# Performance work log

Hardware: AMD Instinct MI355X
Metric: run time of the kernel (lower is better)

The kernel has to match this reference:

```python
import jax, jax.numpy as jnp
import numpy as np

VOCAB = 32000
E = 512      # embed_dim
H = 512      # hidden_dim (== embed_dim, required by the output-averaging slice)
NUM_LAYERS = 2
WIN = 8
S = 512      # seq_len
B = 8        # batch


def setup_inputs() -> dict:
    key = jax.random.key(0)
    ks = jax.random.split(key, 40)
    d = {"encoder_input": jax.random.randint(ks[0], (S, B), 0, VOCAB, dtype=jnp.int64
                                             if jax.config.jax_enable_x64 else jnp.int32)}
    d["embed_table"] = jax.random.normal(ks[1], (VOCAB, E), jnp.float32) * 0.02
    i = 2
    for l in range(NUM_LAYERS):
        in_dim = E if l == 0 else 2 * H
        for dirn in ("f", "b"):
            sc = 1.0 / np.sqrt(H).astype(np.float32)
            d[f"wih{l}{dirn}"] = jax.random.normal(ks[i], (4 * H, in_dim), jnp.float32) * sc; i += 1
            d[f"whh{l}{dirn}"] = jax.random.normal(ks[i], (4 * H, H), jnp.float32) * sc; i += 1
            d[f"b{l}{dirn}"] = jax.random.normal(ks[i], (4 * H,), jnp.float32) * sc; i += 1
    return d


def _lstm_dir(x, mask, wih, whh, b, reverse):
    """One LSTM direction over padded windows. x: [L, N, in], mask: [L, N, 1].
    Masked (out-of-window) steps carry state unchanged; since invalid steps form a
    prefix in scan order (left pad for fwd, right pad for bwd-reversed), the zero
    initial state is preserved until the first valid step -> identical math to
    running the LSTM on the truncated window, as in the original per-token loop."""
    Hh = whh.shape[1]

    def step(carry, inp):
        h, c = carry
        xt, mt = inp
        g = xt @ wih.T + h @ whh.T + b                      # [N, 4H], torch gate order i,f,g,o
        i_, f_, g_, o_ = jnp.split(g, 4, axis=-1)
        c_new = jax.nn.sigmoid(f_) * c + jax.nn.sigmoid(i_) * jnp.tanh(g_)
        h_new = jax.nn.sigmoid(o_) * jnp.tanh(c_new)
        h = jnp.where(mt, h_new, h)
        c = jnp.where(mt, c_new, c)
        return (h, c), h

    N = x.shape[1]
    h0 = jnp.zeros((N, Hh), x.dtype)
    _, ys = jax.lax.scan(step, (h0, h0), (x, mask), reverse=reverse)
    return ys  # [L, N, Hh]


def _forward(encoder_input, embed_table, layer_params):
    S_, B_ = encoder_input.shape
    L = 2 * WIN + 1
    emb = embed_table[encoder_input]                         # [S, B, E]
    offs = jnp.arange(L) - WIN
    pos = jnp.arange(S_)[:, None] + offs[None, :]            # [S, L]
    valid = (pos >= 0) & (pos < S_)
    pidx = jnp.clip(pos, 0, S_ - 1)
    windows = emb[pidx]                                      # [S, L, B, E]
    x = windows.transpose(1, 0, 2, 3).reshape(L, S_ * B_, E)  # [L, N, E]
    mask = jnp.broadcast_to(valid.T[:, :, None, None], (L, S_, B_, 1)).reshape(L, S_ * B_, 1)
    for (wf, hf, bf, wb, hb, bb) in layer_params:
        yf = _lstm_dir(x, mask, wf, hf, bf, reverse=False)
        yb = _lstm_dir(x, mask, wb, hb, bb, reverse=True)
        x = jnp.concatenate([yf, yb], axis=-1)               # [L, N, 2H]
    out = x[WIN].reshape(S_, B_, 2 * H)                      # [S, B, 2H]
    return (out[:, :, :E] + out[:, :, E:]) / 2


def reference(encoder_input, embed_table,
              wih0f, whh0f, b0f, wih0b, whh0b, b0b,
              wih1f, whh1f, b1f, wih1b, whh1b, b1b):
    layer_params = [(wih0f, whh0f, b0f, wih0b, whh0b, b0b),
                    (wih1f, whh1f, b1f, wih1b, whh1b, b1b)]
    return _forward(encoder_input, embed_table, layer_params)
```

## Files before the change

### kernel.cpp

```cpp
#include <hip/hip_runtime.h>
#include <stdint.h>

typedef __bf16 bf16;
typedef __bf16 bf16x8 __attribute__((ext_vector_type(8)));
typedef __bf16 bf16x4 __attribute__((ext_vector_type(4)));
typedef float f32x4 __attribute__((ext_vector_type(4)));

#define WIN 8

__device__ __forceinline__ float sigm(float x) { return 1.0f / (1.0f + __expf(-x)); }
__device__ __forceinline__ float tanhfast(float x) { return 2.0f / (1.0f + __expf(-2.0f * x)) - 1.0f; }

__device__ __forceinline__ void gload16(const void* g, void* l) {
    __builtin_amdgcn_global_load_lds((const __attribute__((address_space(1))) void*)g,
                                     (__attribute__((address_space(3))) void*)l, 16, 0, 0);
}

struct StepArgs {
    const bf16* A1;
    const bf16* A2;
    const bf16* W;
    const float* bias;
    const bf16* P0;
    float* Cst;
    bf16* Hout;
    float* Hf32;
    const bf16* Hprev;
    int l;
    int firstStep;
};

template<int MODE>
__global__ __launch_bounds__(512, 2)
void step_pair(StepArgs fa, StepArgs ba) {
    const StepArgs a = blockIdx.z ? ba : fa;
    __shared__ alignas(16) char lds[131072];

    constexpr int SA1 = (MODE == 0) ? 512 : 1024;
    constexpr int SW  = (MODE == 2) ? 1536 : 512;
    constexpr int SH  = (MODE == 0) ? 2048 : (MODE == 1 ? 1024 : 512);
    constexpr int SHP = (MODE == 1) ? 1024 : 512;

    const int tid = threadIdx.x;
    const int w = tid >> 6;
    const int lane = tid & 63;
    const int wm = w >> 2, wn = w & 3;
    const int bx = blockIdx.x, by = blockIdx.y;
    const int rowBase = bx * 256;

    int KB;
    if (MODE == 0) KB = 8;
    else if (MODE == 1) KB = a.firstStep ? 0 : 8;
    else KB = a.firstStep ? 16 : 24;

    const int lq = lane >> 3;
    const int lc = lane & 7;
    const int swz = 8 * (lc ^ lq);

    const bf16* aP[4];
    const bf16* a2P[4];
    const bf16* bP[4];
#pragma unroll
    for (int q = 0; q < 4; ++q) {
        const int r = w * 32 + q * 8 + lq;
        const int n = rowBase + r;
        aP[q] = a.A1 ? (a.A1 + (size_t)n * SA1 + swz) : (const bf16*)0;
        if (MODE == 2) a2P[q] = a.A2 ? (a.A2 + (size_t)n * 512 + swz) : (const bf16*)0;
        int wr;
        if (MODE == 0) wr = by * 256 + r;
        else wr = ((r & 63) >> 4) * 512 + by * 64 + (r >> 6) * 16 + (r & 15);
        bP[q] = a.W + (size_t)wr * SW + swz;
    }

    const int l15 = lane & 15, l4 = lane >> 4;
    const int key = (l15 & 7) << 4;
    const int aBase = (wm * 128 + l15) * 128;
    const int bBase = (wn * 64 + l15) * 128;

    f32x4 acc[8][4];
    const f32x4 zf = {0.f, 0.f, 0.f, 0.f};
#pragma unroll
    for (int m = 0; m < 8; ++m)
#pragma unroll
        for (int n = 0; n < 4; ++n) acc[m][n] = zf;

    auto STAGE = [&](int buf, int kb) {
        char* Ad = lds + buf * 65536;
        char* Bd = Ad + 32768;
        const int ke = kb * 64;
        const int ldsOff0 = w * 32 * 128;
#pragma unroll
        for (int q = 0; q < 4; ++q) {
            const int ldsOff = ldsOff0 + q * 1024;
            const bf16* srcA;
            if (MODE == 2) srcA = (kb < 16) ? (aP[q] + ke) : (a2P[q] + (ke - 1024));
            else srcA = aP[q] + ke;
            gload16(srcA, Ad + ldsOff);
            gload16(bP[q] + ke, Bd + ldsOff);
        }
    };

    auto LDA4 = [&](bf16x8* d, const char* Ab, int mh, int ko) {
#pragma unroll
        for (int i = 0; i < 4; ++i)
            d[i] = *(const bf16x8*)(Ab + aBase + (mh * 4 + i) * 2048 + ko);
    };
    auto LDB4 = [&](bf16x8* d, const char* Bb, int ko) {
#pragma unroll
        for (int n = 0; n < 4; ++n)
            d[n] = *(const bf16x8*)(Bb + bBase + n * 2048 + ko);
    };
    auto MF16 = [&](const bf16x8* av, const bf16x8* bvv, int mh) {
#pragma unroll
        for (int i = 0; i < 4; ++i)
#pragma unroll
            for (int n = 0; n < 4; ++n)
                acc[mh * 4 + i][n] =
                    __builtin_amdgcn_mfma_f32_16x16x32_bf16(av[i], bvv[n], acc[mh * 4 + i][n], 0, 0, 0);
    };

    if (KB > 0) {
        STAGE(0, 0);
        for (int t = 0; t < KB; ++t) {
            const int cur = t & 1;
            if (t + 1 < KB) {
                STAGE(cur ^ 1, t + 1);
                asm volatile("s_waitcnt vmcnt(8)" ::: "memory");
            } else {
                asm volatile("s_waitcnt vmcnt(0)" ::: "memory");
            }
            __builtin_amdgcn_s_barrier();
            __builtin_amdgcn_sched_barrier(0);
            const char* Ab = lds + cur * 65536;
            const char* Bb = Ab + 32768;
            const int ko0 = (l4 * 16) ^ key;
            const int ko1 = (64 + l4 * 16) ^ key;
            bf16x8 a00[4], a10[4], a01[4], a11[4], b0[4], b1[4];

            LDA4(a00, Ab, 0, ko0); LDB4(b0, Bb, ko0);
            asm volatile("s_waitcnt lgkmcnt(0)" ::: "memory");
            __builtin_amdgcn_sched_barrier(0);
            LDA4(a10, Ab, 0, ko1); LDB4(b1, Bb, ko1);
            __builtin_amdgcn_s_setprio(1);
            MF16(a00, b0, 0);
            __builtin_amdgcn_s_setprio(0);

            asm volatile("s_waitcnt lgkmcnt(0)" ::: "memory");
            __builtin_amdgcn_sched_barrier(0);
            LDA4(a01, Ab, 1, ko0);
            __builtin_amdgcn_s_setprio(1);
            MF16(a10, b1, 0);
            __builtin_amdgcn_s_setprio(0);

            asm volatile("s_waitcnt lgkmcnt(0)" ::: "memory");
            __builtin_amdgcn_sched_barrier(0);
            LDA4(a11, Ab, 1, ko1);
            __builtin_amdgcn_s_setprio(1);
            MF16(a01, b0, 1);
            __builtin_amdgcn_s_setprio(0);

            asm volatile("s_waitcnt lgkmcnt(0)" ::: "memory");
            __builtin_amdgcn_sched_barrier(0);
            __builtin_amdgcn_s_setprio(1);
            MF16(a11, b1, 1);
            __builtin_amdgcn_s_setprio(0);
            __builtin_amdgcn_sched_barrier(0);
            __builtin_amdgcn_s_barrier();
        }
    }

    if (MODE == 0) {
#pragma unroll
        for (int m = 0; m < 8; ++m)
#pragma unroll
            for (int n = 0; n < 4; ++n) {
                const int col = by * 256 + wn * 64 + n * 16 + l15;
#pragma unroll
                for (int e = 0; e < 4; ++e) {
                    const int row = rowBase + wm * 128 + m * 16 + l4 * 4 + e;
                    a.Hout[(size_t)row * SH + col] = (bf16)acc[m][n][e];
                }
            }
        return;
    }

    const int u = by * 64 + wn * 16 + l15;
    const float bi = a.bias[u];
    const float bff = a.bias[512 + u];
    const float bg = a.bias[1024 + u];
    const float bo = a.bias[1536 + u];
#pragma unroll
    for (int m = 0; m < 8; ++m) {
#pragma unroll
        for (int e = 0; e < 4; ++e) {
            const int n = rowBase + wm * 128 + m * 16 + l4 * 4 + e;
            const int s = n >> 3;
            const int p = s + a.l - WIN;
            const bool valid = ((unsigned)p < 512u);
            float gi = acc[m][0][e] + bi;
            float gf = acc[m][1][e] + bff;
            float gg = acc[m][2][e] + bg;
            float go = acc[m][3][e] + bo;
            if (MODE == 1) {
                const int pc = p < 0 ? 0 : (p > 511 ? 511 : p);
                const size_t pr = (size_t)(pc * 8 + (n & 7)) * 2048;
                gi += (float)a.P0[pr + u];
                gf += (float)a.P0[pr + 512 + u];
                gg += (float)a.P0[pr + 1024 + u];
                go += (float)a.P0[pr + 1536 + u];
            }
            const float cold = a.firstStep ? 0.0f : a.Cst[(size_t)n * 512 + u];
            const float cnew = sigm(gf) * cold + sigm(gi) * tanhfast(gg);
            const float hnew = sigm(go) * tanhfast(cnew);
            float hv, cv;
            if (valid) { hv = hnew; cv = cnew; }
            else {
                hv = a.Hprev ? (float)a.Hprev[(size_t)n * SHP + u] : 0.0f;
                cv = cold;
            }
            a.Cst[(size_t)n * 512 + u] = cv;
            a.Hout[(size_t)n * SH + u] = (bf16)hv;
            if (a.Hf32) a.Hf32[(size_t)n * 512 + u] = hv;
        }
    }
}

__global__ void embed_kernel(const int* __restrict__ tok, const float* __restrict__ tbl,
                             bf16* __restrict__ X0) {
    const int n = blockIdx.x;
    const int t = tok[n];
    const float4 v = ((const float4*)(tbl + (size_t)t * 512))[threadIdx.x];
    bf16x4 o = {(bf16)v.x, (bf16)v.y, (bf16)v.z, (bf16)v.w};
    ((bf16x4*)(X0 + (size_t)n * 512))[threadIdx.x] = o;
}

__global__ void cvt_kernel(const float* __restrict__ src, bf16* __restrict__ dst, int n4) {
    const int i = blockIdx.x * 256 + threadIdx.x;
    if (i < n4) {
        const float4 v = ((const float4*)src)[i];
        bf16x4 o = {(bf16)v.x, (bf16)v.y, (bf16)v.z, (bf16)v.w};
        ((bf16x4*)dst)[i] = o;
    }
}

__global__ void build_w1_kernel(const float* __restrict__ wih, const float* __restrict__ whh,
                                bf16* __restrict__ dst) {
    const int r = blockIdx.x;
    for (int k = threadIdx.x; k < 1536; k += 256) {
        const float v = (k < 1024) ? wih[(size_t)r * 1024 + k] : whh[(size_t)r * 512 + (k - 1024)];
        dst[(size_t)r * 1536 + k] = (bf16)v;
    }
}

__global__ void combine_kernel(const float* __restrict__ hf, const float* __restrict__ hb,
                               float* __restrict__ out) {
    const int i = blockIdx.x * 256 + threadIdx.x;
    const float4 x = ((const float4*)hf)[i];
    const float4 y = ((const float4*)hb)[i];
    float4 r;
    r.x = (x.x + y.x) * 0.5f;
    r.y = (x.y + y.y) * 0.5f;
    r.z = (x.z + y.z) * 0.5f;
    r.w = (x.w + y.w) * 0.5f;
    ((float4*)out)[i] = r;
}

extern "C" void kernel_launch(void* const* d_in, const int* in_sizes, int n_in,
                              void* d_out, int out_size, void* d_ws, size_t ws_size,
                              hipStream_t stream) {
    (void)in_sizes; (void)n_in; (void)out_size;
    const int*   tok   = (const int*)d_in[0];
    const float* tbl   = (const float*)d_in[1];
    const float* wih0f = (const float*)d_in[2];
    const float* whh0f = (const float*)d_in[3];
    const float* b0f   = (const float*)d_in[4];
    const float* wih0b = (const float*)d_in[5];
    const float* whh0b = (const float*)d_in[6];
    const float* b0b   = (const float*)d_in[7];
    const float* wih1f = (const float*)d_in[8];
    const float* whh1f = (const float*)d_in[9];
    const float* b1f   = (const float*)d_in[10];
    const float* wih1b = (const float*)d_in[11];
    const float* whh1b = (const float*)d_in[12];
    const float* b1b   = (const float*)d_in[13];

    char* ws = (char*)d_ws;
    size_t off = 0;
    auto alloc = [&](size_t bytes) -> char* {
        char* p = ws + off;
        off += (bytes + 255) & ~(size_t)255;
        return p;
    };
    bf16* wih0f_b = (bf16*)alloc((size_t)2048 * 512 * 2);
    bf16* wih0b_b = (bf16*)alloc((size_t)2048 * 512 * 2);
    bf16* whh0f_b = (bf16*)alloc((size_t)2048 * 512 * 2);
    bf16* whh0b_b = (bf16*)alloc((size_t)2048 * 512 * 2);
    bf16* w1f_b   = (bf16*)alloc((size_t)2048 * 1536 * 2);
    bf16* w1b_b   = (bf16*)alloc((size_t)2048 * 1536 * 2);
    bf16* X0      = (bf16*)alloc((size_t)4096 * 512 * 2);
    bf16* P0f     = (bf16*)alloc((size_t)4096 * 2048 * 2);
    bf16* P0b     = (bf16*)alloc((size_t)4096 * 2048 * 2);
    bf16* X1      = (bf16*)alloc((size_t)17 * 4096 * 1024 * 2);
    float* c0f    = (float*)alloc((size_t)4096 * 512 * 4);
    float* c0b    = (float*)alloc((size_t)4096 * 512 * 4);
    bf16* h1f0    = (bf16*)alloc((size_t)4096 * 512 * 2);
    bf16* h1f1    = (bf16*)alloc((size_t)4096 * 512 * 2);
    bf16* h1b0    = (bf16*)alloc((size_t)4096 * 512 * 2);
    bf16* h1b1    = (bf16*)alloc((size_t)4096 * 512 * 2);
    float* hf32f  = (float*)alloc((size_t)4096 * 512 * 4);
    float* hf32b  = (float*)alloc((size_t)4096 * 512 * 4);
    if (off > ws_size) return;

    bf16* h1f[2] = {h1f0, h1f1};
    bf16* h1b[2] = {h1b0, h1b1};

    cvt_kernel<<<1024, 256, 0, stream>>>(wih0f, wih0f_b, 262144);
    cvt_kernel<<<1024, 256, 0, stream>>>(wih0b, wih0b_b, 262144);
    cvt_kernel<<<1024, 256, 0, stream>>>(whh0f, whh0f_b, 262144);
    cvt_kernel<<<1024, 256, 0, stream>>>(whh0b, whh0b_b, 262144);
    build_w1_kernel<<<2048, 256, 0, stream>>>(wih1f, whh1f, w1f_b);
    build_w1_kernel<<<2048, 256, 0, stream>>>(wih1b, whh1b, w1b_b);
    embed_kernel<<<4096, 128, 0, stream>>>(tok, tbl, X0);

    dim3 g(16, 8, 2), blk(512, 1, 1);

    {
        StepArgs f{}, b{};
        f.A1 = X0; f.W = wih0f_b; f.Hout = P0f;
        b = f; b.W = wih0b_b; b.Hout = P0b;
        step_pair<0><<<g, blk, 0, stream>>>(f, b);
    }

    const size_t SLOT = (size_t)4096 * 1024;

    for (int i = 0; i <= 16; ++i) {
        const int lf = i, lb = 16 - i;
        StepArgs f{}, b{};
        f.A1 = (lf == 0) ? (const bf16*)0 : X1 + (size_t)(lf - 1) * SLOT;
        f.W = whh0f_b; f.bias = b0f; f.P0 = P0f; f.Cst = c0f;
        f.Hout = X1 + (size_t)lf * SLOT; f.Hprev = f.A1;
        f.l = lf; f.firstStep = (lf == 0) ? 1 : 0;
        b.A1 = (lb == 16) ? (const bf16*)0 : X1 + (size_t)(lb + 1) * SLOT + 512;
        b.W = whh0b_b; b.bias = b0b; b.P0 = P0b; b.Cst = c0b;
        b.Hout = X1 + (size_t)lb * SLOT + 512; b.Hprev = b.A1;
        b.l = lb; b.firstStep = (lb == 16) ? 1 : 0;
        step_pair<1><<<g, blk, 0, stream>>>(f, b);
    }

    for (int i = 0; i <= 8; ++i) {
        const int lf = i, lb = 16 - i;
        StepArgs f{}, b{};
        f.A1 = X1 + (size_t)lf * SLOT;
        f.A2 = (i == 0) ? (const bf16*)0 : h1f[(i + 1) & 1];
        f.W = w1f_b; f.bias = b1f; f.Cst = c0f;
        f.Hout = h1f[i & 1]; f.Hf32 = (i == 8) ? hf32f : (float*)0;
        f.Hprev = f.A2;
        f.l = lf; f.firstStep = (i == 0) ? 1 : 0;
        b.A1 = X1 + (size_t)lb * SLOT;
        b.A2 = (i == 0) ? (const bf16*)0 : h1b[(i + 1) & 1];
        b.W = w1b_b; b.bias = b1b; b.Cst = c0b;
        b.Hout = h1b[i & 1]; b.Hf32 = (i == 8) ? hf32b : (float*)0;
        b.Hprev = b.A2;
        b.l = lb; b.firstStep = (i == 0) ? 1 : 0;
        step_pair<2><<<g, blk, 0, stream>>>(f, b);
    }

    combine_kernel<<<2048, 256, 0, stream>>>(hf32f, hf32b, (float*)d_out);
}
```

Before: 1.156 ms.

## Interleave next-tile global-to-LDS prefetch chunks across MFMA phases in GEMM main loop

Splits the per-iteration prefetch of the next K-tile into four chunks issued between the four MFMA phases, instead of one bulk stage followed by a partial wait. Each phase now loads only its own fragments, and the loop waits for all prefetches once at the end of the iteration. The aim is to overlap global loads with compute more evenly and to reduce register pressure from fragment buffers. The cost is extra workgroup barriers in every phase, which may add stalls.

```diff
diff --git a/kernel.cpp b/kernel.cpp
--- a/kernel.cpp
+++ b/kernel.cpp
@@ -84,87 +84,104 @@
 #pragma unroll
         for (int n = 0; n < 4; ++n) acc[m][n] = zf;
 
-    auto STAGE = [&](int buf, int kb) {
-        char* Ad = lds + buf * 65536;
-        char* Bd = Ad + 32768;
+    auto CHUNK = [&](char* Sd, int kb, int q) {
         const int ke = kb * 64;
-        const int ldsOff0 = w * 32 * 128;
-#pragma unroll
-        for (int q = 0; q < 4; ++q) {
-            const int ldsOff = ldsOff0 + q * 1024;
-            const bf16* srcA;
-            if (MODE == 2) srcA = (kb < 16) ? (aP[q] + ke) : (a2P[q] + (ke - 1024));
-            else srcA = aP[q] + ke;
-            gload16(srcA, Ad + ldsOff);
-            gload16(bP[q] + ke, Bd + ldsOff);
-        }
+        const int ldsOff = (w * 32 + q * 8) * 128;
+        const bf16* srcA;
+        if (MODE == 2) srcA = (kb < 16) ? (aP[q] + ke) : (a2P[q] + (ke - 1024));
+        else srcA = aP[q] + ke;
+        gload16(srcA, Sd + ldsOff);
+        gload16(bP[q] + ke, Sd + 32768 + ldsOff);
     };
 
-    auto LDA4 = [&](bf16x8* d, const char* Ab, int mh, int ko) {
-#pragma unroll
-        for (int i = 0; i < 4; ++i)
-            d[i] = *(const bf16x8*)(Ab + aBase + (mh * 4 + i) * 2048 + ko);
-    };
-    auto LDB4 = [&](bf16x8* d, const char* Bb, int ko) {
-#pragma unroll
-        for (int n = 0; n < 4; ++n)
-            d[n] = *(const bf16x8*)(Bb + bBase + n * 2048 + ko);
-    };
-    auto MF16 = [&](const bf16x8* av, const bf16x8* bvv, int mh) {
-#pragma unroll
-        for (int i = 0; i < 4; ++i)
-#pragma unroll
-            for (int n = 0; n < 4; ++n)
-                acc[mh * 4 + i][n] =
-                    __builtin_amdgcn_mfma_f32_16x16x32_bf16(av[i], bvv[n], acc[mh * 4 + i][n], 0, 0, 0);
-    };
-
     if (KB > 0) {
-        STAGE(0, 0);
+#pragma unroll
+        for (int q = 0; q < 4; ++q) CHUNK(lds, 0, q);
+        asm volatile("s_waitcnt vmcnt(0)" ::: "memory");
+        __builtin_amdgcn_s_barrier();
+
         for (int t = 0; t < KB; ++t) {
             const int cur = t & 1;
-            if (t + 1 < KB) {
-                STAGE(cur ^ 1, t + 1);
-                asm volatile("s_waitcnt vmcnt(8)" ::: "memory");
-            } else {
-                asm volatile("s_waitcnt vmcnt(0)" ::: "memory");
-            }
-            __builtin_amdgcn_s_barrier();
-            __builtin_amdgcn_sched_barrier(0);
             const char* Ab = lds + cur * 65536;
             const char* Bb = Ab + 32768;
+            char* Sd = lds + (cur ^ 1) * 65536;
+            const bool pf = (t + 1 < KB);
             const int ko0 = (l4 * 16) ^ key;
             const int ko1 = (64 + l4 * 16) ^ key;
-            bf16x8 a00[4], a10[4], a01[4], a11[4], b0[4], b1[4];
-
-            LDA4(a00, Ab, 0, ko0); LDB4(b0, Bb, ko0);
+            bf16x8 af0[4], af1[4], bv0[4], bv1[4];
+
+            if (pf) { CHUNK(Sd, t + 1, 0); CHUNK(Sd, t + 1, 1); }
+#pragma unroll
+            for (int i = 0; i < 4; ++i)
+                af0[i] = *(const bf16x8*)(Ab + aBase + i * 2048 + ko0);
+#pragma unroll
+            for (int n = 0; n < 4; ++n)
+                bv0[n] = *(const bf16x8*)(Bb + bBase + n * 2048 + ko0);
+            __builtin_amdgcn_s_barrier();
             asm volatile("s_waitcnt lgkmcnt(0)" ::: "memory");
             __builtin_amdgcn_sched_barrier(0);
-            LDA4(a10, Ab, 0, ko1); LDB4(b1, Bb, ko1);
             __builtin_amdgcn_s_setprio(1);
-            MF16(a00, b0, 0);
+#pragma unroll
+            for (int i = 0; i < 4; ++i)
+#pragma unroll
+                for (int n = 0; n < 4; ++n)
+                    acc[i][n] = __builtin_amdgcn_mfma_f32_16x16x32_bf16(af0[i], bv0[n], acc[i][n], 0, 0, 0);
             __builtin_amdgcn_s_setprio(0);
-
+            __builtin_amdgcn_sched_barrier(0);
+            __builtin_amdgcn_s_barrier();
+
+            if (pf) CHUNK(Sd, t + 1, 2);
+#pragma unroll
+            for (int i = 0; i < 4; ++i)
+                af1[i] = *(const bf16x8*)(Ab + aBase + (4 + i) * 2048 + ko0);
+            __builtin_amdgcn_s_barrier();
             asm volatile("s_waitcnt lgkmcnt(0)" ::: "memory");
             __builtin_amdgcn_sched_barrier(0);
-            LDA4(a01, Ab, 1, ko0);
             __builtin_amdgcn_s_setprio(1);
-            MF16(a10, b1, 0);
+#pragma unroll
+            for (int i = 0; i < 4; ++i)
+#pragma unroll
+                for (int n = 0; n < 4; ++n)
+                    acc[4 + i][n] = __builtin_amdgcn_mfma_f32_16x16x32_bf16(af1[i], bv0[n], acc[4 + i][n], 0, 0, 0);
             __builtin_amdgcn_s_setprio(0);
-
+            __builtin_amdgcn_sched_barrier(0);
+            __builtin_amdgcn_s_barrier();
+
+            if (pf) CHUNK(Sd, t + 1, 3);
+#pragma unroll
+            for (int i = 0; i < 4; ++i)
+                af0[i] = *(const bf16x8*)(Ab + aBase + i * 2048 + ko1);
+#pragma unroll
+            for (int n = 0; n < 4; ++n)
+                bv1[n] = *(const bf16x8*)(Bb + bBase + n * 2048 + ko1);
+            __builtin_amdgcn_s_barrier();
             asm volatile("s_waitcnt lgkmcnt(0)" ::: "memory");
             __builtin_amdgcn_sched_barrier(0);
-            LDA4(a11, Ab, 1, ko1);
             __builtin_amdgcn_s_setprio(1);
-            MF16(a01, b0, 1);
+#pragma unroll
+            for (int i = 0; i < 4; ++i)
+#pragma unroll
+                for (int n = 0; n < 4; ++n)
+                    acc[i][n] = __builtin_amdgcn_mfma_f32_16x16x32_bf16(af0[i], bv1[n], acc[i][n], 0, 0, 0);
             __builtin_amdgcn_s_setprio(0);
-
+            __builtin_amdgcn_sched_barrier(0);
+            __builtin_amdgcn_s_barrier();
+
+#pragma unroll
+            for (int i = 0; i < 4; ++i)
+                af1[i] = *(const bf16x8*)(Ab + aBase + (4 + i) * 2048 + ko1);
+            __builtin_amdgcn_s_barrier();
             asm volatile("s_waitcnt lgkmcnt(0)" ::: "memory");
             __builtin_amdgcn_sched_barrier(0);
             __builtin_amdgcn_s_setprio(1);
-            MF16(a11, b1, 1);
+#pragma unroll
+            for (int i = 0; i < 4; ++i)
+#pragma unroll
+                for (int n = 0; n < 4; ++n)
+                    acc[4 + i][n] = __builtin_amdgcn_mfma_f32_16x16x32_bf16(af1[i], bv1[n], acc[4 + i][n], 0, 0, 0);
             __builtin_amdgcn_s_setprio(0);
             __builtin_amdgcn_sched_barrier(0);
+            if (pf) asm volatile("s_waitcnt vmcnt(0)" ::: "memory");
             __builtin_amdgcn_s_barrier();
         }
     }
```

Result: faster. 1.089 ms (-5.8%).
